# Kernel tuning notes

Measured on AMD Instinct MI355X. Metric: run time of the kernel, lower is better.

## Reference

```python
import jax, jax.numpy as jnp
import numpy as np


def rotary_pos_emb(x):
    # x: [b, h, l, k]; interleaved rotary embedding (pairs are (0,1),(2,3),...)
    dim = x.shape[-1]
    seq = x.shape[-2]
    ts = jnp.arange(0, dim, 2, dtype=jnp.float32)
    inv_freqs = 10000.0 ** (-ts / dim)                      # [dim/2]
    grid = jnp.arange(seq, dtype=jnp.float32)[:, None] * inv_freqs[None, :]  # [l, dim/2]
    sin_embs = jnp.repeat(jnp.sin(grid), 2, axis=-1)[None]  # [1, l, dim] (interleaved repeat)
    cos_embs = jnp.repeat(jnp.cos(grid), 2, axis=-1)[None]
    x1, x2 = x[..., ::2], x[..., 1::2]
    xs = jnp.stack([-x2, x1], axis=-1).reshape(x.shape)     # interleave (-x2, x1)
    return x * cos_embs + xs * sin_embs


def setup_inputs() -> dict:
    key = jax.random.key(0)
    ks = jax.random.split(key, 5)
    b, l, d = 2, 2048, 1024
    scale = 1.0 / np.sqrt(d)
    return {
        "x": jax.random.normal(ks[0], (b, l, d), dtype=jnp.float32),
        "Wq": jax.random.normal(ks[1], (d, d), dtype=jnp.float32) * scale,
        "Wk": jax.random.normal(ks[2], (d, d), dtype=jnp.float32) * scale,
        "Wv": jax.random.normal(ks[3], (d, d), dtype=jnp.float32) * scale,
        "Wo": jax.random.normal(ks[4], (d, d), dtype=jnp.float32) * scale,
        "is_training": 0,
    }


def reference(x, Wq, Wk, Wv, Wo, is_training):
    n_heads = 16
    b, l, d = x.shape
    k_size = d // n_heads
    # NOTE: module scales q by 1/sqrt(model_size), not 1/sqrt(key_size)
    q = (x @ Wq) / jnp.sqrt(jnp.float32(d))
    q = q.reshape(b, l, n_heads, k_size).transpose(0, 2, 1, 3)  # b h l k
    k = (x @ Wk).reshape(b, l, n_heads, k_size).transpose(0, 2, 1, 3)
    v = (x @ Wv).reshape(b, l, n_heads, k_size).transpose(0, 2, 1, 3)
    q = rotary_pos_emb(q)
    k = rotary_pos_emb(k)
    logits = jnp.einsum('bhik,bhjk->bhij', q, k)  # no mask, no dropout (eval)
    a = jax.nn.softmax(logits, axis=-1)
    y = jnp.einsum('bhij,bhjv->bhiv', a, v)
    y = y.transpose(0, 2, 1, 3).reshape(b, l, d)  # b l (h v)
    return y @ Wo
```

## Files before the change

### kernel.cpp

```cpp
#include <hip/hip_runtime.h>
#include <stdint.h>

typedef unsigned short u16;
using short8 = __attribute__((ext_vector_type(8))) short;
using f32x4  = __attribute__((ext_vector_type(4))) float;

typedef __attribute__((address_space(1))) unsigned int gu32;
typedef __attribute__((address_space(3))) unsigned int lu32;

__device__ __forceinline__ void gl2lds16(const u16* g, u16* lds_wave_base) {
    __builtin_amdgcn_global_load_lds(
        (gu32*)(uintptr_t)(const void*)g,
        (lu32*)(uint32_t)(uintptr_t)(void*)lds_wave_base,
        16, 0, 0);
}

__device__ inline float bf2f(u16 u) {
    union { unsigned int i; float f; } v;
    v.i = ((unsigned int)u) << 16;
    return v.f;
}
__device__ inline u16 f2bf(float f) {
    union { float f; unsigned int i; } v;
    v.f = f;
    unsigned int x = v.i;
    return (u16)((x + 0x7fffu + ((x >> 16) & 1u)) >> 16);
}
__device__ inline u16 f2bf_trunc(float f) {
    union { float f; unsigned int i; } v;
    v.f = f;
    return (u16)(v.i >> 16);
}

__global__ __launch_bounds__(256) void cvt_x(const float* __restrict__ x,
                                             u16* __restrict__ xb)
{
    int i = (blockIdx.x * 256 + threadIdx.x) * 4;
    float4 v = *(const float4*)(x + i);
    ushort4 o;
    o.x = f2bf(v.x); o.y = f2bf(v.y); o.z = f2bf(v.z); o.w = f2bf(v.w);
    *(ushort4*)(xb + i) = o;
}

__global__ __launch_bounds__(256) void transpose4_cvt(
    const float* __restrict__ w0, const float* __restrict__ w1,
    const float* __restrict__ w2, const float* __restrict__ w3,
    u16* __restrict__ t0, u16* __restrict__ t1,
    u16* __restrict__ t2, u16* __restrict__ t3)
{
    __shared__ u16 tile[32][33];
    const float* src; u16* dst;
    switch (blockIdx.z) {
        case 0:  src = w0; dst = t0; break;
        case 1:  src = w1; dst = t1; break;
        case 2:  src = w2; dst = t2; break;
        default: src = w3; dst = t3; break;
    }
    int tx = threadIdx.x, ty = threadIdx.y;
    int c0 = blockIdx.x * 32, r0 = blockIdx.y * 32;
    #pragma unroll
    for (int i = 0; i < 4; i++)
        tile[ty + i * 8][tx] = f2bf(src[(size_t)(r0 + ty + i * 8) * 1024 + c0 + tx]);
    __syncthreads();
    #pragma unroll
    for (int i = 0; i < 4; i++)
        dst[(size_t)(c0 + ty + i * 8) * 1024 + r0 + tx] = tile[tx][ty + i * 8];
}

__global__ __launch_bounds__(256) void transpose_v(const u16* __restrict__ Vb,
                                                   u16* __restrict__ VT)
{
    __shared__ u16 t[32][33];
    int bh = blockIdx.z, b = bh >> 4, h = bh & 15;
    int p0 = blockIdx.x * 32, c0 = blockIdx.y * 32;
    int tx = threadIdx.x, ty = threadIdx.y;
    #pragma unroll
    for (int i = 0; i < 4; i++)
        t[ty + i * 8][tx] = Vb[(size_t)(b * 2048 + p0 + ty + i * 8) * 1024 + h * 64 + c0 + tx];
    __syncthreads();
    #pragma unroll
    for (int i = 0; i < 4; i++)
        VT[((size_t)bh * 64 + c0 + ty + i * 8) * 2048 + p0 + tx] = t[tx][ty + i * 8];
}

__global__ __launch_bounds__(256) void gemm_qkv(
    const u16* __restrict__ A, const u16* __restrict__ Bt,
    u16* __restrict__ Qb, u16* __restrict__ Kb, u16* __restrict__ Vb)
{
    __shared__ __align__(16) u16 As[128 * 32];
    __shared__ __align__(16) u16 Bs[128 * 32];

    const int tid  = threadIdx.x;
    const int lane = tid & 63;
    const int wid  = tid >> 6;
    const int quad = lane >> 4;
    const int l15  = lane & 15;
    const int wm   = wid >> 1, wn = wid & 1;

    const int m0 = blockIdx.y * 128;
    const int n0 = blockIdx.x * 128;
    const int mat = n0 >> 10;
    const int ln0 = n0 & 1023;
    u16* C = (mat == 0) ? Qb : (mat == 1 ? Kb : Vb);

    f32x4 acc[4][4] = {};

    for (int k0 = 0; k0 < 1024; k0 += 32) {
        #pragma unroll
        for (int it = 0; it < 2; it++) {
            int c   = it * 256 + tid;
            int row = c >> 2;
            int col = ((c & 3) ^ (row & 3)) * 8;
            u16* lbA = &As[(size_t)(it * 256 + wid * 64) * 8];
            u16* lbB = &Bs[(size_t)(it * 256 + wid * 64) * 8];
            gl2lds16(&A [(size_t)(m0 + row) * 1024 + k0 + col], lbA);
            gl2lds16(&Bt[(size_t)(n0 + row) * 1024 + k0 + col], lbB);
        }
        __syncthreads();

        short8 a[4], b[4];
        #pragma unroll
        for (int i = 0; i < 4; i++) {
            int ra = wm * 64 + i * 16 + l15;
            int rb = wn * 64 + i * 16 + l15;
            a[i] = *(const short8*)(&As[ra * 32 + ((quad ^ (ra & 3)) * 8)]);
            b[i] = *(const short8*)(&Bs[rb * 32 + ((quad ^ (rb & 3)) * 8)]);
        }
        #pragma unroll
        for (int i = 0; i < 4; i++)
            #pragma unroll
            for (int j = 0; j < 4; j++)
                acc[i][j] = __builtin_amdgcn_mfma_f32_16x16x32_bf16(a[i], b[j], acc[i][j], 0, 0, 0);
        __syncthreads();
    }

    const float scale = (mat == 0) ? (0.03125f * 1.44269504f) : 1.0f;
    const float l2_10000_over_32 = 0.41524101186f;
    const bool do_rope = (mat < 2);
    const int odd = l15 & 1;

    #pragma unroll
    for (int i = 0; i < 4; i++)
        #pragma unroll
        for (int j = 0; j < 4; j++)
            #pragma unroll
            for (int r = 0; r < 4; r++) {
                int row = m0 + wm * 64 + i * 16 + quad * 4 + r;
                int col = ln0 + wn * 64 + j * 16 + l15;
                float v = acc[i][j][r] * scale;
                float outv;
                if (do_rope) {
                    float vp = __shfl_xor(v, 1);
                    int pi   = (col & 63) >> 1;
                    int pos  = row & 2047;
                    float ang = (float)pos *
                        __builtin_amdgcn_exp2f(-(float)pi * l2_10000_over_32);
                    float sn, cs;
                    __sincosf(ang, &sn, &cs);
                    outv = odd ? (v * cs + vp * sn) : (v * cs - vp * sn);
                } else {
                    outv = v;
                }
                C[(size_t)row * 1024 + col] = f2bf(outv);
            }
}

__global__ __launch_bounds__(256) void gemm_out(
    const u16* __restrict__ A, const u16* __restrict__ Bt, float* __restrict__ C)
{
    __shared__ __align__(16) u16 As[128 * 32];
    __shared__ __align__(16) u16 Bs[128 * 32];

    const int tid  = threadIdx.x;
    const int lane = tid & 63;
    const int wid  = tid >> 6;
    const int quad = lane >> 4;
    const int l15  = lane & 15;
    const int wm   = wid >> 1, wn = wid & 1;

    const int m0 = blockIdx.y * 128;
    const int n0 = blockIdx.x * 128;

    f32x4 acc[4][4] = {};

    for (int k0 = 0; k0 < 1024; k0 += 32) {
        #pragma unroll
        for (int it = 0; it < 2; it++) {
            int c   = it * 256 + tid;
            int row = c >> 2;
            int col = ((c & 3) ^ (row & 3)) * 8;
            u16* lbA = &As[(size_t)(it * 256 + wid * 64) * 8];
            u16* lbB = &Bs[(size_t)(it * 256 + wid * 64) * 8];
            gl2lds16(&A [(size_t)(m0 + row) * 1024 + k0 + col], lbA);
            gl2lds16(&Bt[(size_t)(n0 + row) * 1024 + k0 + col], lbB);
        }
        __syncthreads();

        short8 a[4], b[4];
        #pragma unroll
        for (int i = 0; i < 4; i++) {
            int ra = wm * 64 + i * 16 + l15;
            int rb = wn * 64 + i * 16 + l15;
            a[i] = *(const short8*)(&As[ra * 32 + ((quad ^ (ra & 3)) * 8)]);
            b[i] = *(const short8*)(&Bs[rb * 32 + ((quad ^ (rb & 3)) * 8)]);
        }
        #pragma unroll
        for (int i = 0; i < 4; i++)
            #pragma unroll
            for (int j = 0; j < 4; j++)
                acc[i][j] = __builtin_amdgcn_mfma_f32_16x16x32_bf16(a[i], b[j], acc[i][j], 0, 0, 0);
        __syncthreads();
    }

    #pragma unroll
    for (int i = 0; i < 4; i++)
        #pragma unroll
        for (int j = 0; j < 4; j++)
            #pragma unroll
            for (int r = 0; r < 4; r++) {
                int row = m0 + wm * 64 + i * 16 + quad * 4 + r;
                int col = n0 + wn * 64 + j * 16 + l15;
                C[(size_t)row * 1024 + col] = acc[i][j][r];
            }
}

__global__ __launch_bounds__(256) void attn(
    const u16* __restrict__ Q, const u16* __restrict__ Kb,
    const u16* __restrict__ VT, u16* __restrict__ Y)
{
    __shared__ __align__(16) u16 Ks [128 * 64];
    __shared__ __align__(16) u16 VTs[64 * 128];
    __shared__ __align__(16) u16 Ps [4][16 * 64];

    const int tid  = threadIdx.x;
    const int lane = tid & 63, wid = tid >> 6;
    const int quad = lane >> 4, l15 = lane & 15;

    const int bh = blockIdx.x;
    const int qt = blockIdx.y;
    const int bb = bh >> 4, h = bh & 15;

    const size_t base = ((size_t)bb * 2048) * 1024 + (size_t)h * 64;

    short8 qf[2];
    {
        size_t qrow = (size_t)qt * 64 + wid * 16 + l15;
        const u16* qp = Q + base + qrow * 1024;
        qf[0] = *(const short8*)(qp + quad * 8);
        qf[1] = *(const short8*)(qp + 32 + quad * 8);
    }

    f32x4 o[4] = {};
    float l_r[4] = {0.f, 0.f, 0.f, 0.f};

    for (int j0 = 0; j0 < 2048; j0 += 128) {
        __syncthreads();
        #pragma unroll
        for (int it = 0; it < 4; it++) {
            int c = it * 256 + tid;
            int rk = c >> 3, ck = ((c & 7)  ^ (rk & 7))  * 8;
            int rv = c >> 4, cv = ((c & 15) ^ (rv & 15)) * 8;
            u16* lbK = &Ks [(size_t)(it * 256 + wid * 64) * 8];
            u16* lbV = &VTs[(size_t)(it * 256 + wid * 64) * 8];
            gl2lds16(&Kb[base + (size_t)(j0 + rk) * 1024 + ck], lbK);
            gl2lds16(&VT[((size_t)bh * 64 + rv) * 2048 + j0 + cv], lbV);
        }
        __syncthreads();

        f32x4 s[8];
        #pragma unroll
        for (int nt = 0; nt < 8; nt++) {
            int R = nt * 16 + l15;
            short8 k0 = *(const short8*)(&Ks[R * 64 + (( quad      ^ (R & 7)) * 8)]);
            short8 k1 = *(const short8*)(&Ks[R * 64 + (((quad + 4) ^ (R & 7)) * 8)]);
            f32x4 z = {};
            z = __builtin_amdgcn_mfma_f32_16x16x32_bf16(qf[0], k0, z, 0, 0, 0);
            z = __builtin_amdgcn_mfma_f32_16x16x32_bf16(qf[1], k1, z, 0, 0, 0);
            s[nt] = z;
        }

        #pragma unroll
        for (int hh = 0; hh < 2; hh++) {
            #pragma unroll
            for (int n4 = 0; n4 < 4; n4++) {
                int nt = hh * 4 + n4;
                #pragma unroll
                for (int r = 0; r < 4; r++) {
                    float p = __builtin_amdgcn_exp2f(s[nt][r]);
                    l_r[r] += p;
                    int m = quad * 4 + r;
                    int col = n4 * 16 + l15;
                    Ps[wid][m * 64 + (((col >> 3) ^ (m & 7)) * 8) + (col & 7)]
                        = f2bf_trunc(p);
                }
            }
            asm volatile("s_waitcnt lgkmcnt(0)" ::: "memory");

            short8 pa0 = *(const short8*)(&Ps[wid][l15 * 64 + (( quad      ^ (l15 & 7)) * 8)]);
            short8 pa1 = *(const short8*)(&Ps[wid][l15 * 64 + (((quad + 4) ^ (l15 & 7)) * 8)]);
            #pragma unroll
            for (int nt = 0; nt < 4; nt++) {
                int R = nt * 16 + l15;
                short8 vb0 = *(const short8*)(&VTs[R * 128 + (((hh * 8 + quad)     ^ (R & 15)) * 8)]);
                short8 vb1 = *(const short8*)(&VTs[R * 128 + (((hh * 8 + quad + 4) ^ (R & 15)) * 8)]);
                o[nt] = __builtin_amdgcn_mfma_f32_16x16x32_bf16(pa0, vb0, o[nt], 0, 0, 0);
                o[nt] = __builtin_amdgcn_mfma_f32_16x16x32_bf16(pa1, vb1, o[nt], 0, 0, 0);
            }
            asm volatile("" ::: "memory");
        }
    }

    #pragma unroll
    for (int r = 0; r < 4; r++) {
        l_r[r] += __shfl_xor(l_r[r], 1);
        l_r[r] += __shfl_xor(l_r[r], 2);
        l_r[r] += __shfl_xor(l_r[r], 4);
        l_r[r] += __shfl_xor(l_r[r], 8);
        l_r[r] = 1.0f / l_r[r];
    }

    size_t qrow0 = (size_t)qt * 64 + wid * 16;
    #pragma unroll
    for (int nt = 0; nt < 4; nt++)
        #pragma unroll
        for (int r = 0; r < 4; r++) {
            size_t row = qrow0 + quad * 4 + r;
            Y[base + row * 1024 + nt * 16 + l15] = f2bf(o[nt][r] * l_r[r]);
        }
}

extern "C" void kernel_launch(void* const* d_in, const int* in_sizes, int n_in,
                              void* d_out, int out_size, void* d_ws, size_t ws_size,
                              hipStream_t stream)
{
    const float* x  = (const float*)d_in[0];
    const float* Wq = (const float*)d_in[1];
    const float* Wk = (const float*)d_in[2];
    const float* Wv = (const float*)d_in[3];
    const float* Wo = (const float*)d_in[4];
    float* out = (float*)d_out;

    char* ws = (char*)d_ws;
    u16* xb     = (u16*)(ws + (0ull  << 20));
    u16* WqkvT  = (u16*)(ws + (8ull  << 20));
    u16* WoT    = (u16*)(ws + (14ull << 20));
    u16* Qb     = (u16*)(ws + (16ull << 20));
    u16* Kb     = (u16*)(ws + (24ull << 20));
    u16* Vb     = (u16*)(ws + (32ull << 20));
    u16* VTb    = (u16*)(ws + (40ull << 20));
    u16* Yb     = (u16*)(ws + (48ull << 20));

    cvt_x<<<4096, 256, 0, stream>>>(x, xb);
    transpose4_cvt<<<dim3(32, 32, 4), dim3(32, 8), 0, stream>>>(
        Wq, Wk, Wv, Wo,
        WqkvT, WqkvT + (1024ull * 1024), WqkvT + (2048ull * 1024), WoT);
    gemm_qkv<<<dim3(24, 32), 256, 0, stream>>>(xb, WqkvT, Qb, Kb, Vb);
    transpose_v<<<dim3(64, 2, 32), dim3(32, 8), 0, stream>>>(Vb, VTb);
    attn<<<dim3(32, 32), 256, 0, stream>>>(Qb, Kb, VTb, Yb);
    gemm_out<<<dim3(8, 32), 256, 0, stream>>>(Yb, WoT, out);
}
```

Before: 210.1 us.

## Precompute rope sin/cos table and double attention query tile per block

```diff
diff --git a/kernel.cpp b/kernel.cpp
--- a/kernel.cpp
+++ b/kernel.cpp
@@ -40,6 +40,17 @@
     ushort4 o;
     o.x = f2bf(v.x); o.y = f2bf(v.y); o.z = f2bf(v.z); o.w = f2bf(v.w);
     *(ushort4*)(xb + i) = o;
+}
+
+__global__ __launch_bounds__(256) void rope_tab(float2* __restrict__ tab)
+{
+    int idx = blockIdx.x * 256 + threadIdx.x;
+    int pos = idx >> 5, pi = idx & 31;
+    const float l2_10000_over_32 = 0.41524101186f;
+    float ang = (float)pos * __builtin_amdgcn_exp2f(-(float)pi * l2_10000_over_32);
+    float sn, cs;
+    __sincosf(ang, &sn, &cs);
+    tab[idx] = make_float2(cs, sn);
 }
 
 __global__ __launch_bounds__(256) void transpose4_cvt(
@@ -85,10 +96,12 @@
 
 __global__ __launch_bounds__(256) void gemm_qkv(
     const u16* __restrict__ A, const u16* __restrict__ Bt,
+    const float2* __restrict__ ropetab,
     u16* __restrict__ Qb, u16* __restrict__ Kb, u16* __restrict__ Vb)
 {
     __shared__ __align__(16) u16 As[128 * 32];
     __shared__ __align__(16) u16 Bs[128 * 32];
+    __shared__ float2 scs[128 * 33];
 
     const int tid  = threadIdx.x;
     const int lane = tid & 63;
@@ -102,6 +115,16 @@
     const int mat = n0 >> 10;
     const int ln0 = n0 & 1023;
     u16* C = (mat == 0) ? Qb : (mat == 1 ? Kb : Vb);
+
+    if (mat < 2) {
+        int pos0 = m0 & 2047;
+        #pragma unroll
+        for (int t = 0; t < 16; t++) {
+            int idx = t * 256 + tid;
+            int rr = idx >> 5, pp = idx & 31;
+            scs[rr * 33 + pp] = ropetab[(size_t)(pos0 + rr) * 32 + pp];
+        }
+    }
 
     f32x4 acc[4][4] = {};
 
@@ -135,7 +158,6 @@
     }
 
     const float scale = (mat == 0) ? (0.03125f * 1.44269504f) : 1.0f;
-    const float l2_10000_over_32 = 0.41524101186f;
     const bool do_rope = (mat < 2);
     const int odd = l15 & 1;
 
@@ -145,23 +167,19 @@
         for (int j = 0; j < 4; j++)
             #pragma unroll
             for (int r = 0; r < 4; r++) {
-                int row = m0 + wm * 64 + i * 16 + quad * 4 + r;
-                int col = ln0 + wn * 64 + j * 16 + l15;
+                int lrow = wm * 64 + i * 16 + quad * 4 + r;
+                int col  = ln0 + wn * 64 + j * 16 + l15;
                 float v = acc[i][j][r] * scale;
                 float outv;
                 if (do_rope) {
                     float vp = __shfl_xor(v, 1);
                     int pi   = (col & 63) >> 1;
-                    int pos  = row & 2047;
-                    float ang = (float)pos *
-                        __builtin_amdgcn_exp2f(-(float)pi * l2_10000_over_32);
-                    float sn, cs;
-                    __sincosf(ang, &sn, &cs);
-                    outv = odd ? (v * cs + vp * sn) : (v * cs - vp * sn);
+                    float2 sc = scs[lrow * 33 + pi];
+                    outv = odd ? (v * sc.x + vp * sc.y) : (v * sc.x - vp * sc.y);
                 } else {
                     outv = v;
                 }
-                C[(size_t)row * 1024 + col] = f2bf(outv);
+                C[(size_t)(m0 + lrow) * 1024 + col] = f2bf(outv);
             }
 }
 
@@ -224,13 +242,13 @@
             }
 }
 
-__global__ __launch_bounds__(256) void attn(
+__global__ __launch_bounds__(512) void attn(
     const u16* __restrict__ Q, const u16* __restrict__ Kb,
     const u16* __restrict__ VT, u16* __restrict__ Y)
 {
     __shared__ __align__(16) u16 Ks [128 * 64];
     __shared__ __align__(16) u16 VTs[64 * 128];
-    __shared__ __align__(16) u16 Ps [4][16 * 64];
+    __shared__ __align__(16) u16 Ps [8][16 * 64];
 
     const int tid  = threadIdx.x;
     const int lane = tid & 63, wid = tid >> 6;
@@ -244,7 +262,7 @@
 
     short8 qf[2];
     {
-        size_t qrow = (size_t)qt * 64 + wid * 16 + l15;
+        size_t qrow = (size_t)qt * 128 + wid * 16 + l15;
         const u16* qp = Q + base + qrow * 1024;
         qf[0] = *(const short8*)(qp + quad * 8);
         qf[1] = *(const short8*)(qp + 32 + quad * 8);
@@ -256,12 +274,12 @@
     for (int j0 = 0; j0 < 2048; j0 += 128) {
         __syncthreads();
         #pragma unroll
-        for (int it = 0; it < 4; it++) {
-            int c = it * 256 + tid;
+        for (int it = 0; it < 2; it++) {
+            int c = it * 512 + tid;
             int rk = c >> 3, ck = ((c & 7)  ^ (rk & 7))  * 8;
             int rv = c >> 4, cv = ((c & 15) ^ (rv & 15)) * 8;
-            u16* lbK = &Ks [(size_t)(it * 256 + wid * 64) * 8];
-            u16* lbV = &VTs[(size_t)(it * 256 + wid * 64) * 8];
+            u16* lbK = &Ks [(size_t)(it * 512 + wid * 64) * 8];
+            u16* lbV = &VTs[(size_t)(it * 512 + wid * 64) * 8];
             gl2lds16(&Kb[base + (size_t)(j0 + rk) * 1024 + ck], lbK);
             gl2lds16(&VT[((size_t)bh * 64 + rv) * 2048 + j0 + cv], lbV);
         }
@@ -319,7 +337,7 @@
         l_r[r] = 1.0f / l_r[r];
     }
 
-    size_t qrow0 = (size_t)qt * 64 + wid * 16;
+    size_t qrow0 = (size_t)qt * 128 + wid * 16;
     #pragma unroll
     for (int nt = 0; nt < 4; nt++)
         #pragma unroll
@@ -341,21 +359,23 @@
     float* out = (float*)d_out;
 
     char* ws = (char*)d_ws;
-    u16* xb     = (u16*)(ws + (0ull  << 20));
-    u16* WqkvT  = (u16*)(ws + (8ull  << 20));
-    u16* WoT    = (u16*)(ws + (14ull << 20));
-    u16* Qb     = (u16*)(ws + (16ull << 20));
-    u16* Kb     = (u16*)(ws + (24ull << 20));
-    u16* Vb     = (u16*)(ws + (32ull << 20));
-    u16* VTb    = (u16*)(ws + (40ull << 20));
-    u16* Yb     = (u16*)(ws + (48ull << 20));
+    u16*    xb    = (u16*)   (ws + (0ull  << 20));
+    u16*    WqkvT = (u16*)   (ws + (8ull  << 20));
+    u16*    WoT   = (u16*)   (ws + (14ull << 20));
+    u16*    Qb    = (u16*)   (ws + (16ull << 20));
+    u16*    Kb    = (u16*)   (ws + (24ull << 20));
+    u16*    Vb    = (u16*)   (ws + (32ull << 20));
+    u16*    VTb   = (u16*)   (ws + (40ull << 20));
+    u16*    Yb    = (u16*)   (ws + (48ull << 20));
+    float2* tab   = (float2*)(ws + (56ull << 20));
 
     cvt_x<<<4096, 256, 0, stream>>>(x, xb);
+    rope_tab<<<256, 256, 0, stream>>>(tab);
     transpose4_cvt<<<dim3(32, 32, 4), dim3(32, 8), 0, stream>>>(
         Wq, Wk, Wv, Wo,
         WqkvT, WqkvT + (1024ull * 1024), WqkvT + (2048ull * 1024), WoT);
-    gemm_qkv<<<dim3(24, 32), 256, 0, stream>>>(xb, WqkvT, Qb, Kb, Vb);
+    gemm_qkv<<<dim3(24, 32), 256, 0, stream>>>(xb, WqkvT, tab, Qb, Kb, Vb);
     transpose_v<<<dim3(64, 2, 32), dim3(32, 8), 0, stream>>>(Vb, VTb);
-    attn<<<dim3(32, 32), 256, 0, stream>>>(Qb, Kb, VTb, Yb);
+    attn<<<dim3(32, 16), 512, 0, stream>>>(Qb, Kb, VTb, Yb);
     gemm_out<<<dim3(8, 32), 256, 0, stream>>>(Yb, WoT, out);
 }
```

Result: faster. 205.8 us (-2.0%).
